# Performance work log

Hardware: AMD Instinct MI355X
Metric: run time of the kernel (lower is better)

Reference implementation:

```python
import jax, jax.numpy as jnp
import numpy as np

EPS = 1e-8  # torch CosineSimilarity eps


def setup_inputs() -> dict:
    key = jax.random.key(0)
    k1, k2, k3, k4 = jax.random.split(key, 4)
    N, m, D = 4096, 4, 256
    log_hazard = jax.random.normal(k1, (N,), dtype=jnp.float32)
    encoded_blocks = jax.random.normal(k2, (m, N, D), dtype=jnp.float32)
    time = jax.random.uniform(k3, (N,), dtype=jnp.float32, minval=0.01, maxval=10.0)
    event = jax.random.randint(k4, (N,), 0, 2).astype(jnp.int32)
    M = jnp.asarray(0.1, dtype=jnp.float32)
    return {"log_hazard": log_hazard, "encoded_blocks": encoded_blocks,
            "time": time, "event": event, "M": M}


def _cox_loss(log_hazard, time, event):
    # risk[i, j] = 1 if t_j >= t_i  (equivalent to (outer(t,t) >= t^2).T for t > 0)
    risk = (time[None, :] >= time[:, None]).astype(log_hazard.dtype)
    ev = event.astype(log_hazard.dtype)
    log_risk = jnp.log(risk @ jnp.exp(log_hazard))  # [N]
    return -jnp.sum(ev * (log_hazard - log_risk)) / jnp.sum(ev)


def _similarity_loss(encoded_blocks, M):
    # encoded_blocks: [m, N, D]
    m, N, D = encoded_blocks.shape
    norms = jnp.maximum(jnp.linalg.norm(encoded_blocks, axis=-1, keepdims=True), EPS)
    xn = encoded_blocks / norms                         # normalized embeddings [m,N,D]
    S = jnp.einsum('mid,mjd->mij', xn, xn)              # pairwise cosine sims [m,N,N]
    # modality is 'missing' for a patient if all features equal the first feature
    missing = jnp.all(encoded_blocks == encoded_blocks[..., :1], axis=-1)  # [m,N]
    valid = (~missing[:, :, None] & ~missing[:, None, :]).astype(S.dtype)  # [m,N,N]
    self_sim = jnp.diagonal(S, axis1=1, axis2=2)        # cos(x_i, x_i) per modality [m,N]
    psim = jnp.sum(valid * self_sim[:, :, None], axis=0)  # [N,N] patient self-similarity
    msim = jnp.sum(valid * S, axis=0)                     # [N,N] matched similarity
    offdiag = 1.0 - jnp.eye(N, dtype=S.dtype)
    return jnp.sum(offdiag * jax.nn.relu(M - msim + psim))


def reference(log_hazard, encoded_blocks, time, event, M):
    cox = _cox_loss(log_hazard, time, event)
    sim = _similarity_loss(encoded_blocks, M)
    return cox + sim
```

## Files before the change

### kernel.cpp

```cpp
#include <hip/hip_runtime.h>

#define N_PAT 4096
#define NMOD  4
#define OFFPAIRS 16773120.0

__global__ __launch_bounds__(256) void prep_cox_kernel(
    const float* __restrict__ eb, const float* __restrict__ h,
    const float* __restrict__ t, const int* __restrict__ ev,
    float* __restrict__ part_v, float* __restrict__ part_D,
    float* __restrict__ part_n, float* __restrict__ num_part,
    float* __restrict__ den_part, int* __restrict__ ctr)
{
  __shared__ float shmem[8192];
  __shared__ float rsh[8];
  int tid = threadIdx.x;
  int wid = tid >> 6, lane = tid & 63;
  int b = blockIdx.x;

  if (b < 1024) {
    if (b == 0 && tid == 0) *ctr = 0;
    float* xsh = shmem;
    float* dsh = shmem + 1024;
    float* nsh = shmem + 1028;
    float4 acc = {0.f, 0.f, 0.f, 0.f};
    float Dacc = 0.f, nacc = 0.f;
#pragma unroll
    for (int rr = 0; rr < 4; ++rr) {
      int row = b * 16 + wid * 4 + rr;
      const float* base = eb + (size_t)row * 256;
      float4 v = *(const float4*)(base + lane * 4);
      float x0 = base[0];
      int eq = (v.x == x0) & (v.y == x0) & (v.z == x0) & (v.w == x0);
      float ss = v.x * v.x + v.y * v.y + v.z * v.z + v.w * v.w;
#pragma unroll
      for (int o = 32; o; o >>= 1) ss += __shfl_xor(ss, o, 64);
      int missing = __all(eq);
      float denom = fmaxf(sqrtf(ss), 1e-8f);
      float inv = missing ? 0.0f : (1.0f / denom);
      acc.x += v.x * inv; acc.y += v.y * inv;
      acc.z += v.z * inv; acc.w += v.w * inv;
      Dacc += missing ? 0.0f : (ss * inv * inv);
      nacc += missing ? 0.0f : 1.0f;
    }
    xsh[wid * 256 + lane * 4 + 0] = acc.x;
    xsh[wid * 256 + lane * 4 + 1] = acc.y;
    xsh[wid * 256 + lane * 4 + 2] = acc.z;
    xsh[wid * 256 + lane * 4 + 3] = acc.w;
    if (lane == 0) { dsh[wid] = Dacc; nsh[wid] = nacc; }
    __syncthreads();
    part_v[(size_t)b * 256 + tid] =
        (xsh[tid] + xsh[256 + tid]) + (xsh[512 + tid] + xsh[768 + tid]);
    if (tid == 0) part_D[b] = (dsh[0] + dsh[1]) + (dsh[2] + dsh[3]);
    if (tid == 1) part_n[b] = (nsh[0] + nsh[1]) + (nsh[2] + nsh[3]);
  } else {
    float* tl = shmem;
    float* el = shmem + 4096;
    for (int q = tid; q < N_PAT; q += 256) {
      tl[q] = t[q];
      el[q] = expf(h[q]);
    }
    __syncthreads();
    int cb = b - 1024;
    float numw = 0.f, denw = 0.f;
#pragma unroll
    for (int r = 0; r < 4; ++r) {
      int i = cb * 16 + wid * 4 + r;
      float ti = tl[i];
      float s = 0.f;
#pragma unroll
      for (int it = 0; it < 16; ++it) {
        int j = (it * 64 + lane) * 4;
        float4 tv = *(const float4*)(&tl[j]);
        float4 evv = *(const float4*)(&el[j]);
        s += (tv.x >= ti) ? evv.x : 0.f;
        s += (tv.y >= ti) ? evv.y : 0.f;
        s += (tv.z >= ti) ? evv.z : 0.f;
        s += (tv.w >= ti) ? evv.w : 0.f;
      }
#pragma unroll
      for (int o = 32; o; o >>= 1) s += __shfl_xor(s, o, 64);
      if (lane == 0) {
        float e = (float)ev[i];
        numw += e * (h[i] - logf(s));
        denw += e;
      }
    }
    if (lane == 0) { rsh[wid] = numw; rsh[4 + wid] = denw; }
    __syncthreads();
    if (tid == 0) num_part[cb] = (rsh[0] + rsh[1]) + (rsh[2] + rsh[3]);
    if (tid == 1) den_part[cb] = (rsh[4] + rsh[5]) + (rsh[6] + rsh[7]);
  }
}

__global__ __launch_bounds__(256) void reduce_finalize_kernel(
    const float* __restrict__ part_v, const float* __restrict__ part_D,
    const float* __restrict__ part_n, const float* __restrict__ num_part,
    const float* __restrict__ den_part, const float* __restrict__ Mp,
    float* __restrict__ vsq_part, float* __restrict__ D_part16,
    float* __restrict__ n_part16, float* __restrict__ num16,
    float* __restrict__ den16, int* __restrict__ ctr,
    float* __restrict__ out)
{
  __shared__ float vsh[4][64];
  __shared__ int lastflag;
  int tid = threadIdx.x, lane = tid & 63, wid = tid >> 6;
  int g = blockIdx.x;
  int m = g >> 2, dq = g & 3;

  int d = dq * 64 + lane;
  const float* vb = part_v + ((size_t)(m * 256 + wid * 64)) * 256 + d;
  float s = 0.f;
#pragma unroll 8
  for (int r = 0; r < 64; ++r) s += vb[(size_t)r * 256];
  vsh[wid][lane] = s;
  __syncthreads();

  if (wid == 0) {
    float vd = (vsh[0][lane] + vsh[1][lane]) + (vsh[2][lane] + vsh[3][lane]);
    float vsq = vd * vd;
    float Dv = part_D[g * 64 + lane];
    float nv = part_n[g * 64 + lane];
    float nm = (lane < 16) ? num_part[g * 16 + lane] : 0.f;
    float dn = (lane < 16) ? den_part[g * 16 + lane] : 0.f;
#pragma unroll
    for (int o = 32; o; o >>= 1) {
      vsq += __shfl_xor(vsq, o, 64);
      Dv  += __shfl_xor(Dv, o, 64);
      nv  += __shfl_xor(nv, o, 64);
      nm  += __shfl_xor(nm, o, 64);
      dn  += __shfl_xor(dn, o, 64);
    }
    if (lane == 0) {
      vsq_part[g] = vsq;
      D_part16[g] = Dv;
      n_part16[g] = nv;
      num16[g]    = nm;
      den16[g]    = dn;
    }
  }
  __syncthreads();
  if (tid == 0) {
    __threadfence();
    int prev = __hip_atomic_fetch_add(ctr, 1, __ATOMIC_ACQ_REL,
                                      __HIP_MEMORY_SCOPE_AGENT);
    lastflag = (prev == 15);
  }
  __syncthreads();

  if (lastflag && tid == 0) {
    __threadfence();
    double sim = (double)Mp[0] * OFFPAIRS;
    for (int mm = 0; mm < NMOD; ++mm) {
      double Dm = 0.0, nmm = 0.0;
      for (int q = 0; q < 4; ++q) {
        Dm  += (double)D_part16[mm * 4 + q];
        nmm += (double)n_part16[mm * 4 + q];
      }
      sim += nmm * Dm;
    }
    for (int q = 0; q < 16; ++q) sim -= (double)vsq_part[q];
    double n = 0.0, dd = 0.0;
    for (int q = 0; q < 16; ++q) { n += (double)num16[q]; dd += (double)den16[q]; }
    out[0] = (float)(-n / dd + sim);
  }
}

extern "C" void kernel_launch(void* const* d_in, const int* in_sizes, int n_in,
                              void* d_out, int out_size, void* d_ws, size_t ws_size,
                              hipStream_t stream)
{
  const float* h  = (const float*)d_in[0];
  const float* eb = (const float*)d_in[1];
  const float* tm = (const float*)d_in[2];
  const int*   ev = (const int*)d_in[3];
  const float* Mp = (const float*)d_in[4];
  float* out = (float*)d_out;

  char* ws = (char*)d_ws;
  float* part_v   = (float*)ws;
  float* part_D   = part_v + 1024 * 256;
  float* part_n   = part_D + 1024;
  float* num_part = part_n + 1024;
  float* den_part = num_part + 256;
  float* vsq_part = den_part + 256;
  float* D_part16 = vsq_part + 16;
  float* n_part16 = D_part16 + 16;
  float* num16    = n_part16 + 16;
  float* den16    = num16 + 16;
  int*   ctr      = (int*)(den16 + 16);

  prep_cox_kernel<<<dim3(1280), dim3(256), 0, stream>>>(
      eb, h, tm, ev, part_v, part_D, part_n, num_part, den_part, ctr);
  reduce_finalize_kernel<<<dim3(16), dim3(256), 0, stream>>>(
      part_v, part_D, part_n, num_part, den_part, Mp,
      vsq_part, D_part16, n_part16, num16, den16, ctr, out);
}
```

Baseline: 19.61 us.

## Schedule cox blocks first, keep times in registers, widen final reduction grid

The heavier Cox risk-sum blocks now take the low block indices so they are dispatched before the cheap normalization blocks. Each thread now holds its slice of the time vector in registers instead of staging it in shared memory, which halves the LDS footprint to 16 KB and should allow more resident blocks per CU. The second kernel is split across 64 blocks instead of 16, with shorter per-thread column sums, to spread the part_v reduction over more CUs. The costs are higher register pressure from the 16 float4 time values and more atomic and partial-sum traffic in the final reduction.

```diff
diff --git a/kernel.cpp b/kernel.cpp
--- a/kernel.cpp
+++ b/kernel.cpp
@@ -11,22 +11,56 @@
     float* __restrict__ part_n, float* __restrict__ num_part,
     float* __restrict__ den_part, int* __restrict__ ctr)
 {
-  __shared__ float shmem[8192];
-  __shared__ float rsh[8];
+  __shared__ float shmem[4096];
+  __shared__ float dsh[4], nsh[4], rsh[8];
   int tid = threadIdx.x;
   int wid = tid >> 6, lane = tid & 63;
   int b = blockIdx.x;
 
-  if (b < 1024) {
+  if (b < 256) {
     if (b == 0 && tid == 0) *ctr = 0;
+    float* el = shmem;
+    for (int q = tid; q < N_PAT; q += 256) el[q] = expf(h[q]);
+    float4 tv[16];
+#pragma unroll
+    for (int it = 0; it < 16; ++it)
+      tv[it] = *(const float4*)(t + (it * 64 + lane) * 4);
+    __syncthreads();
+
+    float numw = 0.f, denw = 0.f;
+#pragma unroll
+    for (int r = 0; r < 4; ++r) {
+      int i = b * 16 + wid * 4 + r;
+      float ti = t[i];
+      float s = 0.f;
+#pragma unroll
+      for (int it = 0; it < 16; ++it) {
+        float4 evv = *(const float4*)(&el[(it * 64 + lane) * 4]);
+        s += (tv[it].x >= ti) ? evv.x : 0.f;
+        s += (tv[it].y >= ti) ? evv.y : 0.f;
+        s += (tv[it].z >= ti) ? evv.z : 0.f;
+        s += (tv[it].w >= ti) ? evv.w : 0.f;
+      }
+#pragma unroll
+      for (int o = 32; o; o >>= 1) s += __shfl_xor(s, o, 64);
+      if (lane == 0) {
+        float e = (float)ev[i];
+        numw += e * (h[i] - logf(s));
+        denw += e;
+      }
+    }
+    if (lane == 0) { rsh[wid] = numw; rsh[4 + wid] = denw; }
+    __syncthreads();
+    if (tid == 0) num_part[b] = (rsh[0] + rsh[1]) + (rsh[2] + rsh[3]);
+    if (tid == 1) den_part[b] = (rsh[4] + rsh[5]) + (rsh[6] + rsh[7]);
+  } else {
+    int pb = b - 256;
     float* xsh = shmem;
-    float* dsh = shmem + 1024;
-    float* nsh = shmem + 1028;
     float4 acc = {0.f, 0.f, 0.f, 0.f};
     float Dacc = 0.f, nacc = 0.f;
 #pragma unroll
     for (int rr = 0; rr < 4; ++rr) {
-      int row = b * 16 + wid * 4 + rr;
+      int row = pb * 16 + wid * 4 + rr;
       const float* base = eb + (size_t)row * 256;
       float4 v = *(const float4*)(base + lane * 4);
       float x0 = base[0];
@@ -48,47 +82,10 @@
     xsh[wid * 256 + lane * 4 + 3] = acc.w;
     if (lane == 0) { dsh[wid] = Dacc; nsh[wid] = nacc; }
     __syncthreads();
-    part_v[(size_t)b * 256 + tid] =
+    part_v[(size_t)pb * 256 + tid] =
         (xsh[tid] + xsh[256 + tid]) + (xsh[512 + tid] + xsh[768 + tid]);
-    if (tid == 0) part_D[b] = (dsh[0] + dsh[1]) + (dsh[2] + dsh[3]);
-    if (tid == 1) part_n[b] = (nsh[0] + nsh[1]) + (nsh[2] + nsh[3]);
-  } else {
-    float* tl = shmem;
-    float* el = shmem + 4096;
-    for (int q = tid; q < N_PAT; q += 256) {
-      tl[q] = t[q];
-      el[q] = expf(h[q]);
-    }
-    __syncthreads();
-    int cb = b - 1024;
-    float numw = 0.f, denw = 0.f;
-#pragma unroll
-    for (int r = 0; r < 4; ++r) {
-      int i = cb * 16 + wid * 4 + r;
-      float ti = tl[i];
-      float s = 0.f;
-#pragma unroll
-      for (int it = 0; it < 16; ++it) {
-        int j = (it * 64 + lane) * 4;
-        float4 tv = *(const float4*)(&tl[j]);
-        float4 evv = *(const float4*)(&el[j]);
-        s += (tv.x >= ti) ? evv.x : 0.f;
-        s += (tv.y >= ti) ? evv.y : 0.f;
-        s += (tv.z >= ti) ? evv.z : 0.f;
-        s += (tv.w >= ti) ? evv.w : 0.f;
-      }
-#pragma unroll
-      for (int o = 32; o; o >>= 1) s += __shfl_xor(s, o, 64);
-      if (lane == 0) {
-        float e = (float)ev[i];
-        numw += e * (h[i] - logf(s));
-        denw += e;
-      }
-    }
-    if (lane == 0) { rsh[wid] = numw; rsh[4 + wid] = denw; }
-    __syncthreads();
-    if (tid == 0) num_part[cb] = (rsh[0] + rsh[1]) + (rsh[2] + rsh[3]);
-    if (tid == 1) den_part[cb] = (rsh[4] + rsh[5]) + (rsh[6] + rsh[7]);
+    if (tid == 0) part_D[pb] = (dsh[0] + dsh[1]) + (dsh[2] + dsh[3]);
+    if (tid == 1) part_n[pb] = (nsh[0] + nsh[1]) + (nsh[2] + nsh[3]);
   }
 }
 
@@ -96,46 +93,46 @@
     const float* __restrict__ part_v, const float* __restrict__ part_D,
     const float* __restrict__ part_n, const float* __restrict__ num_part,
     const float* __restrict__ den_part, const float* __restrict__ Mp,
-    float* __restrict__ vsq_part, float* __restrict__ D_part16,
-    float* __restrict__ n_part16, float* __restrict__ num16,
-    float* __restrict__ den16, int* __restrict__ ctr,
+    float* __restrict__ vsq64, float* __restrict__ D64,
+    float* __restrict__ n64, float* __restrict__ num64,
+    float* __restrict__ den64, int* __restrict__ ctr,
     float* __restrict__ out)
 {
-  __shared__ float vsh[4][64];
+  __shared__ float vsh[16][16];
   __shared__ int lastflag;
-  int tid = threadIdx.x, lane = tid & 63, wid = tid >> 6;
+  int tid = threadIdx.x;
   int g = blockIdx.x;
-  int m = g >> 2, dq = g & 3;
+  int m = g >> 4, cq = g & 15;
+  int rc = tid >> 4, c = tid & 15;
 
-  int d = dq * 64 + lane;
-  const float* vb = part_v + ((size_t)(m * 256 + wid * 64)) * 256 + d;
-  float s = 0.f;
-#pragma unroll 8
-  for (int r = 0; r < 64; ++r) s += vb[(size_t)r * 256];
-  vsh[wid][lane] = s;
+  {
+    const float* vb = part_v + ((size_t)(m * 256 + rc * 16)) * 256 + cq * 16 + c;
+    float s = 0.f;
+#pragma unroll
+    for (int k = 0; k < 16; ++k) s += vb[k * 256];
+    vsh[rc][c] = s;
+  }
   __syncthreads();
 
-  if (wid == 0) {
-    float vd = (vsh[0][lane] + vsh[1][lane]) + (vsh[2][lane] + vsh[3][lane]);
+  if (tid < 16) {
+    float vd = 0.f;
+#pragma unroll
+    for (int k = 0; k < 16; ++k) vd += vsh[k][tid];
     float vsq = vd * vd;
-    float Dv = part_D[g * 64 + lane];
-    float nv = part_n[g * 64 + lane];
-    float nm = (lane < 16) ? num_part[g * 16 + lane] : 0.f;
-    float dn = (lane < 16) ? den_part[g * 16 + lane] : 0.f;
+    float Dv = part_D[g * 16 + tid];
+    float nv = part_n[g * 16 + tid];
+    float nm = (tid < 4) ? num_part[g * 4 + tid] : 0.f;
+    float dn = (tid < 4) ? den_part[g * 4 + tid] : 0.f;
 #pragma unroll
-    for (int o = 32; o; o >>= 1) {
+    for (int o = 8; o; o >>= 1) {
       vsq += __shfl_xor(vsq, o, 64);
       Dv  += __shfl_xor(Dv, o, 64);
       nv  += __shfl_xor(nv, o, 64);
       nm  += __shfl_xor(nm, o, 64);
       dn  += __shfl_xor(dn, o, 64);
     }
-    if (lane == 0) {
-      vsq_part[g] = vsq;
-      D_part16[g] = Dv;
-      n_part16[g] = nv;
-      num16[g]    = nm;
-      den16[g]    = dn;
+    if (tid == 0) {
+      vsq64[g] = vsq; D64[g] = Dv; n64[g] = nv; num64[g] = nm; den64[g] = dn;
     }
   }
   __syncthreads();
@@ -143,7 +140,7 @@
     __threadfence();
     int prev = __hip_atomic_fetch_add(ctr, 1, __ATOMIC_ACQ_REL,
                                       __HIP_MEMORY_SCOPE_AGENT);
-    lastflag = (prev == 15);
+    lastflag = (prev == 63);
   }
   __syncthreads();
 
@@ -152,15 +149,15 @@
     double sim = (double)Mp[0] * OFFPAIRS;
     for (int mm = 0; mm < NMOD; ++mm) {
       double Dm = 0.0, nmm = 0.0;
-      for (int q = 0; q < 4; ++q) {
-        Dm  += (double)D_part16[mm * 4 + q];
-        nmm += (double)n_part16[mm * 4 + q];
+      for (int q = 0; q < 16; ++q) {
+        Dm  += (double)D64[mm * 16 + q];
+        nmm += (double)n64[mm * 16 + q];
       }
       sim += nmm * Dm;
     }
-    for (int q = 0; q < 16; ++q) sim -= (double)vsq_part[q];
+    for (int q = 0; q < 64; ++q) sim -= (double)vsq64[q];
     double n = 0.0, dd = 0.0;
-    for (int q = 0; q < 16; ++q) { n += (double)num16[q]; dd += (double)den16[q]; }
+    for (int q = 0; q < 64; ++q) { n += (double)num64[q]; dd += (double)den64[q]; }
     out[0] = (float)(-n / dd + sim);
   }
 }
@@ -182,16 +179,16 @@
   float* part_n   = part_D + 1024;
   float* num_part = part_n + 1024;
   float* den_part = num_part + 256;
-  float* vsq_part = den_part + 256;
-  float* D_part16 = vsq_part + 16;
-  float* n_part16 = D_part16 + 16;
-  float* num16    = n_part16 + 16;
-  float* den16    = num16 + 16;
-  int*   ctr      = (int*)(den16 + 16);
+  float* vsq64    = den_part + 256;
+  float* D64      = vsq64 + 64;
+  float* n64      = D64 + 64;
+  float* num64    = n64 + 64;
+  float* den64    = num64 + 64;
+  int*   ctr      = (int*)(den64 + 64);
 
   prep_cox_kernel<<<dim3(1280), dim3(256), 0, stream>>>(
       eb, h, tm, ev, part_v, part_D, part_n, num_part, den_part, ctr);
-  reduce_finalize_kernel<<<dim3(16), dim3(256), 0, stream>>>(
+  reduce_finalize_kernel<<<dim3(64), dim3(256), 0, stream>>>(
       part_v, part_D, part_n, num_part, den_part, Mp,
-      vsq_part, D_part16, n_part16, num16, den16, ctr, out);
+      vsq64, D64, n64, num64, den64, ctr, out);
 }
```

Result: slower. 21.53 us (+9.8%).
